# Kernel tuning notes

Hardware: AMD Instinct MI355X
Metric: run time of the kernel (lower is better)

## Reference

```python
import jax, jax.numpy as jnp
import numpy as np

INPUT_SIZE = 224
B, C, H, W = 256, 3, 256, 256
KSIZE = 15
KHALF = KSIZE // 2


def setup_inputs() -> dict:
    key = jax.random.key(0)
    x = jax.random.uniform(key, (B, C, H, W), dtype=jnp.float32)
    return {"x": x}


def _rgb_to_hsv(img):  # img [B,3,Hs,Ws] -> (h,s,v) each [B,Hs,Ws]
    r, g, b = img[:, 0], img[:, 1], img[:, 2]
    maxc = jnp.maximum(jnp.maximum(r, g), b)
    minc = jnp.minimum(jnp.minimum(r, g), b)
    v = maxc
    d = maxc - minc
    s = jnp.where(maxc > 0, d / jnp.where(maxc > 0, maxc, 1.0), 0.0)
    dn = jnp.where(d > 0, d, 1.0)
    rc, gc, bc = (maxc - r) / dn, (maxc - g) / dn, (maxc - b) / dn
    h = jnp.where(maxc == r, bc - gc, jnp.where(maxc == g, 2.0 + rc - bc, 4.0 + gc - rc))
    h = jnp.where(d > 0, (h / 6.0) % 1.0, 0.0)
    return h, s, v


def _hsv_to_rgb(h, s, v):  # -> [B,3,Hs,Ws]
    i = jnp.floor(h * 6.0)
    f = h * 6.0 - i
    i = i.astype(jnp.int32) % 6
    p = v * (1.0 - s)
    q = v * (1.0 - s * f)
    t = v * (1.0 - s * (1.0 - f))
    conds = [i == 0, i == 1, i == 2, i == 3, i == 4, i == 5]
    r = jnp.select(conds, [v, q, p, p, t, v])
    g = jnp.select(conds, [t, v, v, q, p, p])
    b = jnp.select(conds, [p, p, t, v, v, q])
    return jnp.stack([r, g, b], axis=1)


def _gray(img):  # ITU-R 601 luma, keep channel dim
    w = jnp.array([0.2989, 0.587, 0.114], dtype=img.dtype).reshape(1, 3, 1, 1)
    return jnp.sum(img * w, axis=1, keepdims=True)


def _blur_axis(img, kern, axis):
    # img [B,C,S,S]; kern [B,KSIZE]; separable 1D gaussian along `axis` with reflect pad
    pad = [(0, 0)] * 4
    pad[axis] = (KHALF, KHALF)
    xp = jnp.pad(img, pad, mode='reflect')
    out = jnp.zeros_like(img)
    S = img.shape[axis]
    for k in range(KSIZE):  # fixed small loop, fuses under jit
        sl = jax.lax.slice_in_dim(xp, k, k + S, axis=axis)
        out = out + kern[:, k].reshape(B, 1, 1, 1) * sl
    return out


def _pipeline(x):
    key = jax.random.key(42)
    ks = jax.random.split(key, 10)

    # ---- RandomResizedCrop(scale=(0.8,1.0), ratio=(3/4,4/3), bicubic) ----
    area = (H * W) * jax.random.uniform(ks[0], (B,), minval=0.8, maxval=1.0)
    ratio = jnp.exp(jax.random.uniform(ks[1], (B,), minval=np.log(3.0 / 4.0), maxval=np.log(4.0 / 3.0)))
    cw = jnp.clip(jnp.round(jnp.sqrt(area * ratio)), 1.0, float(W))
    ch = jnp.clip(jnp.round(jnp.sqrt(area / ratio)), 1.0, float(H))
    i0 = jnp.floor(jax.random.uniform(ks[2], (B,)) * (H - ch + 1.0))
    j0 = jnp.floor(jax.random.uniform(ks[3], (B,)) * (W - cw + 1.0))
    sy, sx = INPUT_SIZE / ch, INPUT_SIZE / cw
    ty, tx = -i0 * sy, -j0 * sx

    def crop_resize(img, scale, trans):
        return jax.image.scale_and_translate(
            img, (C, INPUT_SIZE, INPUT_SIZE), (1, 2), scale, trans,
            method='cubic', antialias=True)

    xc = jax.vmap(crop_resize)(x, jnp.stack([sy, sx], -1), jnp.stack([ty, tx], -1))

    # ---- ColorJitter(0.1, 0.1, 0.1, 0.01), RandomApply p=0.8 ----
    bf = jax.random.uniform(ks[4], (B, 1, 1, 1), minval=0.9, maxval=1.1)
    cf = jax.random.uniform(ks[5], (B, 1, 1, 1), minval=0.9, maxval=1.1)
    sf = jax.random.uniform(ks[6], (B, 1, 1, 1), minval=0.9, maxval=1.1)
    hf = jax.random.uniform(ks[7], (B, 1, 1), minval=-0.01, maxval=0.01)

    xj = jnp.clip(xc * bf, 0.0, 1.0)                                      # brightness
    mean_gray = jnp.mean(_gray(xj), axis=(2, 3), keepdims=True)
    xj = jnp.clip(cf * xj + (1.0 - cf) * mean_gray, 0.0, 1.0)             # contrast
    xj = jnp.clip(sf * xj + (1.0 - sf) * _gray(xj), 0.0, 1.0)             # saturation
    h, s, v = _rgb_to_hsv(xj)                                             # hue
    xj = _hsv_to_rgb((h + hf) % 1.0, s, v)

    apply_cj = (jax.random.uniform(ks[8], (B, 1, 1, 1)) < 0.8)
    xj = jnp.where(apply_cj, xj, xc)

    # ---- GaussianBlur(kernel_size=15, sigma~U(0.1,2.0)), RandomApply p=0.5 ----
    kb = jax.random.split(ks[9], 2)
    sigma = jax.random.uniform(kb[0], (B,), minval=0.1, maxval=2.0)
    t = jnp.arange(KSIZE, dtype=jnp.float32) - KHALF
    kern = jnp.exp(-0.5 * (t[None, :] / sigma[:, None]) ** 2)
    kern = kern / jnp.sum(kern, axis=1, keepdims=True)                    # [B,15]
    xb = _blur_axis(_blur_axis(xj, kern, 2), kern, 3)
    apply_bl = (jax.random.uniform(kb[1], (B, 1, 1, 1)) < 0.5)
    return jnp.where(apply_bl, xb, xj)


def reference(x):
    return _pipeline(x)
```

## Files before the change

kernel.cpp:

```cpp
#include <hip/hip_runtime.h>
#include <cstdint>
#include <cstddef>


#define JAX_PARTITIONABLE 1

#define NB 256
#define NC 3
#define IH 256
#define IW 256
#define OS 224
#define PIX (OS * OS)
#define PSTRIDE 32
#define TROWS 16
#define LROWS 24
#define NTILE 14
#define CSTRIDE 28
#define YSTR 25

__device__ __forceinline__ float bf2f(unsigned short u) {
  return __uint_as_float(((unsigned)u) << 16);
}
__device__ __forceinline__ unsigned short f2bf(float f) {
  unsigned u = __float_as_uint(f);
  return (unsigned short)((u + 0x7FFFu + ((u >> 16) & 1u)) >> 16);
}

__device__ __forceinline__ void tf2x32(uint32_t k0, uint32_t k1,
                                       uint32_t x0, uint32_t x1,
                                       uint32_t& o0, uint32_t& o1) {
  uint32_t ks[3] = {k0, k1, k0 ^ k1 ^ 0x1BD11BDAu};
  uint32_t a = x0 + ks[0], b = x1 + ks[1];
  const int R[2][4] = {{13, 15, 26, 6}, {17, 29, 16, 24}};
  #pragma unroll
  for (int i = 0; i < 5; ++i) {
    #pragma unroll
    for (int j = 0; j < 4; ++j) {
      int r = R[i & 1][j];
      a += b;
      b = (b << r) | (b >> (32 - r));
      b ^= a;
    }
    a += ks[(i + 1) % 3];
    b += ks[(i + 2) % 3] + (uint32_t)(i + 1);
  }
  o0 = a; o1 = b;
}

__device__ __forceinline__ float bits_to_u01(uint32_t bits) {
  uint32_t fb = (bits >> 9) | 0x3f800000u;
  return __uint_as_float(fb) - 1.0f;
}

__device__ __forceinline__ float u01_n(uint32_t k0, uint32_t k1, uint32_t i, uint32_t N) {
#if JAX_PARTITIONABLE
  uint32_t a, b; tf2x32(k0, k1, 0u, i, a, b);
  return bits_to_u01(a ^ b);
#else
  uint32_t half = N >> 1;
  uint32_t a, b;
  if (i < half) { tf2x32(k0, k1, i, half + i, a, b); return bits_to_u01(a); }
  tf2x32(k0, k1, i - half, i, a, b); return bits_to_u01(b);
#endif
}

__device__ __forceinline__ float junif(uint32_t k0, uint32_t k1, uint32_t i, uint32_t N,
                                       float mn, float mx) {
  float u = u01_n(k0, k1, i, N);
  float d = __fsub_rn(mx, mn);
  float r = __fadd_rn(__fmul_rn(u, d), mn);
  return fmaxf(mn, r);
}

__global__ __launch_bounds__(256) void k_params(float* __restrict__ prm) {
  int b = threadIdx.x;
  if (b >= NB) return;
  uint32_t ks[10][2];
#if JAX_PARTITIONABLE
  for (int j = 0; j < 10; ++j) tf2x32(0u, 42u, 0u, (uint32_t)j, ks[j][0], ks[j][1]);
#else
  {
    uint32_t flat[20];
    for (int j = 0; j < 10; ++j) {
      uint32_t a, bb; tf2x32(0u, 42u, (uint32_t)j, (uint32_t)(10 + j), a, bb);
      flat[j] = a; flat[10 + j] = bb;
    }
    for (int j = 0; j < 10; ++j) { ks[j][0] = flat[2 * j]; ks[j][1] = flat[2 * j + 1]; }
  }
#endif
  float* P = prm + b * PSTRIDE;

  float uarea = junif(ks[0][0], ks[0][1], b, NB, 0.8f, 1.0f);
  float area  = __fmul_rn(65536.0f, uarea);
  float lmn = (float)(-0.28768207245178085);
  float lmx = (float)( 0.28768207245178085);
  float ur  = junif(ks[1][0], ks[1][1], b, NB, lmn, lmx);
  float ratio = (float)exp((double)ur);

  float cw = rintf(__fsqrt_rn(__fmul_rn(area, ratio)));
  cw = fminf(fmaxf(cw, 1.0f), 256.0f);
  float ch = rintf(__fsqrt_rn(__fdiv_rn(area, ratio)));
  ch = fminf(fmaxf(ch, 1.0f), 256.0f);

  float ui = u01_n(ks[2][0], ks[2][1], b, NB);
  float uj = u01_n(ks[3][0], ks[3][1], b, NB);
  float i0 = floorf(__fmul_rn(ui, __fadd_rn(__fsub_rn(256.0f, ch), 1.0f)));
  float j0 = floorf(__fmul_rn(uj, __fadd_rn(__fsub_rn(256.0f, cw), 1.0f)));

  float sy = __fdiv_rn(224.0f, ch), sx = __fdiv_rn(224.0f, cw);
  float ty = -__fmul_rn(i0, sy),   tx = -__fmul_rn(j0, sx);
  float inv_sy = __fdiv_rn(1.0f, sy), inv_sx = __fdiv_rn(1.0f, sx);
  P[0] = inv_sy;
  P[1] = __fmul_rn(ty, inv_sy);
  P[2] = fmaxf(inv_sy, 1.0f);
  P[3] = inv_sx;
  P[4] = __fmul_rn(tx, inv_sx);
  P[5] = fmaxf(inv_sx, 1.0f);

  P[6] = junif(ks[4][0], ks[4][1], b, NB, 0.9f, 1.1f);
  P[7] = junif(ks[5][0], ks[5][1], b, NB, 0.9f, 1.1f);
  P[8] = junif(ks[6][0], ks[6][1], b, NB, 0.9f, 1.1f);
  P[9] = junif(ks[7][0], ks[7][1], b, NB, -0.01f, 0.01f);
  P[10] = (u01_n(ks[8][0], ks[8][1], b, NB) < 0.8f) ? 1.0f : 0.0f;

  uint32_t kb0[2], kb1[2];
#if JAX_PARTITIONABLE
  tf2x32(ks[9][0], ks[9][1], 0u, 0u, kb0[0], kb0[1]);
  tf2x32(ks[9][0], ks[9][1], 0u, 1u, kb1[0], kb1[1]);
#else
  {
    uint32_t f0, s0, f1, s1;
    tf2x32(ks[9][0], ks[9][1], 0u, 2u, f0, s0);
    tf2x32(ks[9][0], ks[9][1], 1u, 3u, f1, s1);
    kb0[0] = f0; kb0[1] = f1; kb1[0] = s0; kb1[1] = s1;
  }
#endif
  float sg = junif(kb0[0], kb0[1], b, NB, 0.1f, 2.0f);
  P[11] = (u01_n(kb1[0], kb1[1], b, NB) < 0.5f) ? 1.0f : 0.0f;

  float e[15]; float ssum = 0.0f;
  for (int k = 0; k < 15; ++k) {
    float t = (float)k - 7.0f;
    float z = t / sg;
    e[k] = expf(-0.5f * (z * z));
    ssum += e[k];
  }
  for (int k = 0; k < 15; ++k) P[12 + k] = e[k] / ssum;
}

__device__ __forceinline__ float keys_cubic(float x) {
  float o = ((1.5f * x - 2.5f) * x) * x + 1.0f;
  if (x >= 1.0f) o = ((-0.5f * x + 2.5f) * x - 4.0f) * x + 2.0f;
  if (x >= 2.0f) o = 0.0f;
  return o;
}

__global__ __launch_bounds__(224) void k_weights(const float* __restrict__ prm,
                                                 float* __restrict__ wtab) {
  int o = threadIdx.x;
  int dim = blockIdx.x & 1;
  int b = blockIdx.x >> 1;
  const float* P = prm + b * PSTRIDE;
  float inv = dim ? P[3] : P[0];
  float ti  = dim ? P[4] : P[1];
  float ks  = dim ? P[5] : P[2];
  float sf = ((float)o + 0.5f) * inv - ti - 0.5f;
  float r = 2.0f * ks;
  int i0 = max(0, (int)ceilf(sf - r));
  int i1 = min(255, (int)floorf(sf + r));
  int n = i1 - i0 + 1; if (n > 6) n = 6;
  float w[6]; float tot = 0.0f;
  #pragma unroll
  for (int j = 0; j < 6; ++j) {
    float v = 0.0f;
    if (j < n) { float d = fabsf(sf - (float)(i0 + j)) / ks; v = keys_cubic(d); }
    w[j] = v; tot += v;
  }
  float ri = (fabsf(tot) > 1.1920929e-4f) ? (1.0f / tot) : 0.0f;
  float* W = wtab + ((size_t)(b * 2 + dim) * 224 + o) * 8;
  #pragma unroll
  for (int j = 0; j < 6; ++j) W[j] = w[j] * ri;
  W[6] = (float)i0;
  W[7] = (float)n;
}

__global__ __launch_bounds__(256) void k_resize(const float* __restrict__ x,
                                                float* __restrict__ xc,
                                                float* __restrict__ rowsum,
                                                const float* __restrict__ prm,
                                                const float* __restrict__ wtab) {
  int blk = blockIdx.x;
  int tile = blk % NTILE;
  int c = (blk / NTILE) % NC;
  int b = blk / (NTILE * NC);
  int t = threadIdx.x;
  int oyb = tile * TROWS;
  const float* P = prm + b * PSTRIDE;
  const float* wty = wtab + ((size_t)(b * 2) * 224 + oyb) * 8;

  __shared__ __align__(16) float s_mem[256 * CSTRIDE];
  __shared__ __align__(16) float s_wyl[TROWS * 8];
  __shared__ float wsum[4];

  if (t < TROWS * 8) s_wyl[t] = wty[t];

  int base = (int)wty[6];

  {
    const float* src = x + (size_t)(b * NC + c) * IH * IW + t;
    float* colp = s_mem + t * CSTRIDE;
    #pragma unroll
    for (int k = 0; k < 6; ++k) {
      float4 v;
      v.x = src[(size_t)min(base + 4 * k + 0, IH - 1) * IW];
      v.y = src[(size_t)min(base + 4 * k + 1, IH - 1) * IW];
      v.z = src[(size_t)min(base + 4 * k + 2, IH - 1) * IW];
      v.w = src[(size_t)min(base + 4 * k + 3, IH - 1) * IW];
      *(float4*)(colp + 4 * k) = v;
    }
  }
  __syncthreads();

  float xr[LROWS];
  #pragma unroll
  for (int r = 0; r < LROWS; ++r) xr[r] = 0.0f;
  if (t < OS) {
    const float4* W4 = (const float4*)(wtab + ((size_t)(b * 2 + 1) * 224 + t) * 8);
    float4 wA = W4[0], wB = W4[1];
    int ix0 = (int)wB.z;
    #pragma unroll
    for (int j = 0; j < 6; ++j) {
      float wj = (j == 0) ? wA.x : (j == 1) ? wA.y : (j == 2) ? wA.z
               : (j == 3) ? wA.w : (j == 4) ? wB.x : wB.y;
      const float* colp = s_mem + (ix0 + j) * CSTRIDE;
      #pragma unroll
      for (int k = 0; k < 6; ++k) {
        float4 f = *(const float4*)(colp + 4 * k);
        xr[4 * k + 0] += wj * f.x;
        xr[4 * k + 1] += wj * f.y;
        xr[4 * k + 2] += wj * f.z;
        xr[4 * k + 3] += wj * f.w;
      }
    }
  }
  __syncthreads();

  {
    float* colq = s_mem + t * YSTR;
    #pragma unroll
    for (int r = 0; r < LROWS; ++r) colq[r] = xr[r];
  }
  __syncthreads();

  float bfac = P[6];
  float psum = 0.0f;
  bool act = (t < OS);
  float* dst = xc + ((size_t)(b * NC + c) * OS + oyb) * OS + t;
  const float* colq = s_mem + t * YSTR;
  #pragma unroll 2
  for (int i = 0; i < TROWS; ++i) {
    float4 a = *(const float4*)&s_wyl[i * 8];
    float4 h = *(const float4*)&s_wyl[i * 8 + 4];
    int ry0 = (int)h.z - base;
    const float* p = colq + ry0;
    float acc = a.x * p[0] + a.y * p[1] + a.z * p[2]
              + a.w * p[3] + h.x * p[4] + h.y * p[5];
    if (act) {
      dst[(size_t)i * OS] = acc;
      psum += fminf(fmaxf(acc * bfac, 0.0f), 1.0f);
    }
  }
  for (int off = 32; off > 0; off >>= 1) psum += __shfl_down(psum, off, 64);
  int wid = t >> 6, lane = t & 63;
  if (lane == 0) wsum[wid] = psum;
  __syncthreads();
  if (t == 0) rowsum[blk] = wsum[0] + wsum[1] + wsum[2] + wsum[3];
}

__global__ __launch_bounds__(64) void k_means(const float* __restrict__ rowsum,
                                              float* __restrict__ means) {
  int b = blockIdx.x, t = threadIdx.x;
  float acc = 0.0f;
  if (t < NC * NTILE) {
    int c = t / NTILE;
    float w = (c == 0) ? 0.2989f : ((c == 1) ? 0.587f : 0.114f);
    acc = w * rowsum[b * NC * NTILE + t];
  }
  for (int off = 32; off > 0; off >>= 1) acc += __shfl_down(acc, off, 64);
  if (t == 0) means[b] = acc / (float)PIX;
}

__device__ __forceinline__ float clip01(float x) { return fminf(fmaxf(x, 0.0f), 1.0f); }
__device__ __forceinline__ float fmod1(float x)  { return x - floorf(x); }

__device__ __forceinline__ void jitter_px(float& r, float& g, float& bb,
                                          float mg, float bfac, float cfac,
                                          float sfac, float hfac) {
  r = clip01(r * bfac); g = clip01(g * bfac); bb = clip01(bb * bfac);
  r  = clip01(cfac * r  + (1.0f - cfac) * mg);
  g  = clip01(cfac * g  + (1.0f - cfac) * mg);
  bb = clip01(cfac * bb + (1.0f - cfac) * mg);
  float gray = 0.2989f * r + 0.587f * g + 0.114f * bb;
  r  = clip01(sfac * r  + (1.0f - sfac) * gray);
  g  = clip01(sfac * g  + (1.0f - sfac) * gray);
  bb = clip01(sfac * bb + (1.0f - sfac) * gray);
  float maxc = fmaxf(r, fmaxf(g, bb));
  float minc = fminf(r, fminf(g, bb));
  float v = maxc, d = maxc - minc;
  float s = (maxc > 0.0f) ? (d / maxc) : 0.0f;
  float dn = (d > 0.0f) ? d : 1.0f;
  float rc = (maxc - r) / dn, gc = (maxc - g) / dn, bc2 = (maxc - bb) / dn;
  float h = (maxc == r) ? (bc2 - gc)
          : ((maxc == g) ? (2.0f + rc - bc2) : (4.0f + gc - rc));
  h = (d > 0.0f) ? fmod1(h / 6.0f) : 0.0f;
  h = fmod1(h + hfac);
  float fi = floorf(h * 6.0f);
  float f = h * 6.0f - fi;
  int i = ((int)fi) % 6;
  float pp = v * (1.0f - s);
  float q  = v * (1.0f - s * f);
  float tt = v * (1.0f - s * (1.0f - f));
  switch (i) {
    case 0: r = v;  g = tt; bb = pp; break;
    case 1: r = q;  g = v;  bb = pp; break;
    case 2: r = pp; g = v;  bb = tt; break;
    case 3: r = pp; g = q;  bb = v;  break;
    case 4: r = tt; g = pp; bb = v;  break;
    default: r = v; g = pp; bb = q;  break;
  }
}

__global__ __launch_bounds__(256) void k_jitter(const float* __restrict__ xc,
                                                const float* __restrict__ means,
                                                const float* __restrict__ prm,
                                                unsigned short* __restrict__ xjb,
                                                float* __restrict__ out) {
  int idx = blockIdx.x * 256 + threadIdx.x;
  const int QPB = PIX / 4;
  if (idx >= NB * QPB) return;
  int b = idx / QPB, p4 = idx - b * QPB;
  const float* P = prm + b * PSTRIDE;
  float bfac = P[6], cfac = P[7], sfac = P[8], hfac = P[9];
  bool cj = P[10] != 0.0f;
  bool bl = P[11] != 0.0f;
  size_t base4 = ((size_t)b * NC * PIX) / 4 + p4;
  const float4* in4 = (const float4*)xc;
  float4 r4 = in4[base4];
  float4 g4 = in4[base4 + PIX / 4];
  float4 b4 = in4[base4 + 2 * (PIX / 4)];
  if (cj) {
    float mg = means[b];
    float* rp = (float*)&r4; float* gp = (float*)&g4; float* bp = (float*)&b4;
    #pragma unroll
    for (int k = 0; k < 4; ++k) jitter_px(rp[k], gp[k], bp[k], mg, bfac, cfac, sfac, hfac);
  }
  if (bl) {
    ushort4* dst = (ushort4*)xjb;
    ushort4 s;
    s.x = f2bf(r4.x); s.y = f2bf(r4.y); s.z = f2bf(r4.z); s.w = f2bf(r4.w);
    dst[base4] = s;
    s.x = f2bf(g4.x); s.y = f2bf(g4.y); s.z = f2bf(g4.z); s.w = f2bf(g4.w);
    dst[base4 + PIX / 4] = s;
    s.x = f2bf(b4.x); s.y = f2bf(b4.y); s.z = f2bf(b4.z); s.w = f2bf(b4.w);
    dst[base4 + 2 * (PIX / 4)] = s;
  } else {
    float4* dst4 = (float4*)out;
    dst4[base4] = r4;
    dst4[base4 + PIX / 4] = g4;
    dst4[base4 + 2 * (PIX / 4)] = b4;
  }
}

__global__ __launch_bounds__(256) void k_blur(const unsigned short* __restrict__ xjb,
                                              float* __restrict__ out,
                                              const float* __restrict__ prm) {
  int blk = blockIdx.x;
  int tile = blk % NTILE;
  int c = (blk / NTILE) % NC;
  int b = blk / (NTILE * NC);
  const float* P = prm + b * PSTRIDE;
  if (P[11] == 0.0f) return;
  int t = threadIdx.x;
  int oyb = tile * TROWS;

  __shared__ float s_in[TROWS + 14][OS];
  __shared__ float s_mid[TROWS][OS];
  __shared__ float s_k[15];
  if (t < 15) s_k[t] = P[12 + t];

  const ushort4* plane4 = (const ushort4*)(xjb + (size_t)(b * NC + c) * PIX);
  float* oplane = out + (size_t)(b * NC + c) * PIX;
  {
    float4* s4 = (float4*)&s_in[0][0];
    const int RQ = OS / 4;
    for (int f = t; f < (TROWS + 14) * RQ; f += 256) {
      int r = f / RQ, col4 = f - r * RQ;
      int yy = oyb - 7 + r;
      yy = (yy < 0) ? -yy : ((yy > OS - 1) ? (2 * (OS - 1) - yy) : yy);
      ushort4 q = plane4[yy * RQ + col4];
      s4[f] = make_float4(bf2f(q.x), bf2f(q.y), bf2f(q.z), bf2f(q.w));
    }
  }
  __syncthreads();
  if (t < OS) {
    for (int i = 0; i < TROWS; ++i) {
      float acc = 0.0f;
      #pragma unroll
      for (int k = 0; k < 15; ++k) acc += s_k[k] * s_in[i + k][t];
      s_mid[i][t] = acc;
    }
  }
  __syncthreads();
  if (t < OS) {
    for (int i = 0; i < TROWS; ++i) {
      float acc = 0.0f;
      #pragma unroll
      for (int k = 0; k < 15; ++k) {
        int xx = t - 7 + k;
        xx = (xx < 0) ? -xx : ((xx > OS - 1) ? (2 * (OS - 1) - xx) : xx);
        acc += s_k[k] * s_mid[i][xx];
      }
      oplane[(size_t)(oyb + i) * OS + t] = acc;
    }
  }
}

extern "C" void kernel_launch(void* const* d_in, const int* in_sizes, int n_in,
                              void* d_out, int out_size, void* d_ws, size_t ws_size,
                              hipStream_t stream) {
  const float* x = (const float*)d_in[0];
  float* out = (float*)d_out;
  char* ws = (char*)d_ws;

  float* prm    = (float*)ws;
  float* rowsum = (float*)(ws + 32768);
  float* means  = (float*)(ws + 75776);
  float* wtab   = (float*)(ws + 76800);
  unsigned short* xjb = (unsigned short*)(ws + 3746816);

  k_params<<<1, 256, 0, stream>>>(prm);
  k_weights<<<NB * 2, 224, 0, stream>>>(prm, wtab);

  int nblk = NB * NC * NTILE;
  k_resize<<<nblk, 256, 0, stream>>>(x, out, rowsum, prm, wtab);
  k_means<<<NB, 64, 0, stream>>>(rowsum, means);

  int nquad = NB * (PIX / 4);
  k_jitter<<<(nquad + 255) / 256, 256, 0, stream>>>(out, means, prm, xjb, out);

  k_blur<<<nblk, 256, 0, stream>>>(xjb, out, prm);
}
```

Measured before the change: 197.1 us.

## Store resized crop in bf16 and jitter in place to cut intermediate traffic

```diff
diff --git a/kernel.cpp b/kernel.cpp
--- a/kernel.cpp
+++ b/kernel.cpp
@@ -185,7 +185,7 @@
 }
 
 __global__ __launch_bounds__(256) void k_resize(const float* __restrict__ x,
-                                                float* __restrict__ xc,
+                                                unsigned short* __restrict__ xcj,
                                                 float* __restrict__ rowsum,
                                                 const float* __restrict__ prm,
                                                 const float* __restrict__ wtab) {
@@ -255,7 +255,7 @@
   float bfac = P[6];
   float psum = 0.0f;
   bool act = (t < OS);
-  float* dst = xc + ((size_t)(b * NC + c) * OS + oyb) * OS + t;
+  unsigned short* dst = xcj + ((size_t)(b * NC + c) * OS + oyb) * OS + t;
   const float* colq = s_mem + t * YSTR;
   #pragma unroll 2
   for (int i = 0; i < TROWS; ++i) {
@@ -266,7 +266,7 @@
     float acc = a.x * p[0] + a.y * p[1] + a.z * p[2]
               + a.w * p[3] + h.x * p[4] + h.y * p[5];
     if (act) {
-      dst[(size_t)i * OS] = acc;
+      dst[(size_t)i * OS] = f2bf(acc);
       psum += fminf(fmaxf(acc * bfac, 0.0f), 1.0f);
     }
   }
@@ -330,10 +330,9 @@
   }
 }
 
-__global__ __launch_bounds__(256) void k_jitter(const float* __restrict__ xc,
+__global__ __launch_bounds__(256) void k_jitter(unsigned short* __restrict__ xcj,
                                                 const float* __restrict__ means,
                                                 const float* __restrict__ prm,
-                                                unsigned short* __restrict__ xjb,
                                                 float* __restrict__ out) {
   int idx = blockIdx.x * 256 + threadIdx.x;
   const int QPB = PIX / 4;
@@ -343,11 +342,15 @@
   float bfac = P[6], cfac = P[7], sfac = P[8], hfac = P[9];
   bool cj = P[10] != 0.0f;
   bool bl = P[11] != 0.0f;
+  if (bl && !cj) return;
   size_t base4 = ((size_t)b * NC * PIX) / 4 + p4;
-  const float4* in4 = (const float4*)xc;
-  float4 r4 = in4[base4];
-  float4 g4 = in4[base4 + PIX / 4];
-  float4 b4 = in4[base4 + 2 * (PIX / 4)];
+  ushort4* in4 = (ushort4*)xcj;
+  ushort4 ru = in4[base4];
+  ushort4 gu = in4[base4 + PIX / 4];
+  ushort4 bu = in4[base4 + 2 * (PIX / 4)];
+  float4 r4 = make_float4(bf2f(ru.x), bf2f(ru.y), bf2f(ru.z), bf2f(ru.w));
+  float4 g4 = make_float4(bf2f(gu.x), bf2f(gu.y), bf2f(gu.z), bf2f(gu.w));
+  float4 b4 = make_float4(bf2f(bu.x), bf2f(bu.y), bf2f(bu.z), bf2f(bu.w));
   if (cj) {
     float mg = means[b];
     float* rp = (float*)&r4; float* gp = (float*)&g4; float* bp = (float*)&b4;
@@ -355,14 +358,13 @@
     for (int k = 0; k < 4; ++k) jitter_px(rp[k], gp[k], bp[k], mg, bfac, cfac, sfac, hfac);
   }
   if (bl) {
-    ushort4* dst = (ushort4*)xjb;
     ushort4 s;
     s.x = f2bf(r4.x); s.y = f2bf(r4.y); s.z = f2bf(r4.z); s.w = f2bf(r4.w);
-    dst[base4] = s;
+    in4[base4] = s;
     s.x = f2bf(g4.x); s.y = f2bf(g4.y); s.z = f2bf(g4.z); s.w = f2bf(g4.w);
-    dst[base4 + PIX / 4] = s;
+    in4[base4 + PIX / 4] = s;
     s.x = f2bf(b4.x); s.y = f2bf(b4.y); s.z = f2bf(b4.z); s.w = f2bf(b4.w);
-    dst[base4 + 2 * (PIX / 4)] = s;
+    in4[base4 + 2 * (PIX / 4)] = s;
   } else {
     float4* dst4 = (float4*)out;
     dst4[base4] = r4;
@@ -371,7 +373,7 @@
   }
 }
 
-__global__ __launch_bounds__(256) void k_blur(const unsigned short* __restrict__ xjb,
+__global__ __launch_bounds__(256) void k_blur(const unsigned short* __restrict__ xcj,
                                               float* __restrict__ out,
                                               const float* __restrict__ prm) {
   int blk = blockIdx.x;
@@ -383,44 +385,56 @@
   int t = threadIdx.x;
   int oyb = tile * TROWS;
 
-  __shared__ float s_in[TROWS + 14][OS];
-  __shared__ float s_mid[TROWS][OS];
+  __shared__ unsigned short s_in[TROWS + 14][228];
+  __shared__ float s_mid[TROWS][226];
   __shared__ float s_k[15];
   if (t < 15) s_k[t] = P[12 + t];
 
-  const ushort4* plane4 = (const ushort4*)(xjb + (size_t)(b * NC + c) * PIX);
+  const unsigned short* plane = xcj + (size_t)(b * NC + c) * PIX;
   float* oplane = out + (size_t)(b * NC + c) * PIX;
+
   {
-    float4* s4 = (float4*)&s_in[0][0];
     const int RQ = OS / 4;
     for (int f = t; f < (TROWS + 14) * RQ; f += 256) {
-      int r = f / RQ, col4 = f - r * RQ;
+      int r = f / RQ, q = f - r * RQ;
       int yy = oyb - 7 + r;
       yy = (yy < 0) ? -yy : ((yy > OS - 1) ? (2 * (OS - 1) - yy) : yy);
-      ushort4 q = plane4[yy * RQ + col4];
-      s4[f] = make_float4(bf2f(q.x), bf2f(q.y), bf2f(q.z), bf2f(q.w));
-    }
-  }
-  __syncthreads();
+      *(ushort4*)&s_in[r][4 * q] = *(const ushort4*)(plane + (size_t)yy * OS + 4 * q);
+    }
+  }
+  __syncthreads();
+
+  float w[15];
+  #pragma unroll
+  for (int k = 0; k < 15; ++k) w[k] = s_k[k];
+
+  float acc[TROWS];
+  #pragma unroll
+  for (int i = 0; i < TROWS; ++i) acc[i] = 0.0f;
+  if (t < OS) {
+    #pragma unroll
+    for (int r = 0; r < TROWS + 14; ++r) {
+      float val = bf2f(s_in[r][t]);
+      #pragma unroll
+      for (int i = 0; i < TROWS; ++i) {
+        if (i <= r && r - i <= 14) acc[i] += w[r - i] * val;
+      }
+    }
+    #pragma unroll
+    for (int i = 0; i < TROWS; ++i) s_mid[i][t] = acc[i];
+  }
+  __syncthreads();
+
   if (t < OS) {
     for (int i = 0; i < TROWS; ++i) {
-      float acc = 0.0f;
-      #pragma unroll
-      for (int k = 0; k < 15; ++k) acc += s_k[k] * s_in[i + k][t];
-      s_mid[i][t] = acc;
-    }
-  }
-  __syncthreads();
-  if (t < OS) {
-    for (int i = 0; i < TROWS; ++i) {
-      float acc = 0.0f;
+      float a2 = 0.0f;
       #pragma unroll
       for (int k = 0; k < 15; ++k) {
         int xx = t - 7 + k;
         xx = (xx < 0) ? -xx : ((xx > OS - 1) ? (2 * (OS - 1) - xx) : xx);
-        acc += s_k[k] * s_mid[i][xx];
+        a2 += w[k] * s_mid[i][xx];
       }
-      oplane[(size_t)(oyb + i) * OS + t] = acc;
+      oplane[(size_t)(oyb + i) * OS + t] = a2;
     }
   }
 }
@@ -436,17 +450,17 @@
   float* rowsum = (float*)(ws + 32768);
   float* means  = (float*)(ws + 75776);
   float* wtab   = (float*)(ws + 76800);
-  unsigned short* xjb = (unsigned short*)(ws + 3746816);
+  unsigned short* xcj = (unsigned short*)(ws + 3746816);
 
   k_params<<<1, 256, 0, stream>>>(prm);
   k_weights<<<NB * 2, 224, 0, stream>>>(prm, wtab);
 
   int nblk = NB * NC * NTILE;
-  k_resize<<<nblk, 256, 0, stream>>>(x, out, rowsum, prm, wtab);
+  k_resize<<<nblk, 256, 0, stream>>>(x, xcj, rowsum, prm, wtab);
   k_means<<<NB, 64, 0, stream>>>(rowsum, means);
 
   int nquad = NB * (PIX / 4);
-  k_jitter<<<(nquad + 255) / 256, 256, 0, stream>>>(out, means, prm, xjb, out);
-
-  k_blur<<<nblk, 256, 0, stream>>>(xjb, out, prm);
-}
+  k_jitter<<<(nquad + 255) / 256, 256, 0, stream>>>(xcj, means, prm, out);
+
+  k_blur<<<nblk, 256, 0, stream>>>(xcj, out, prm);
+}
```

Measured after the change: 170.8 us (median of 2 runs). -13.3%, faster.
